# Performance work log

Hardware: AMD Instinct MI355X
Metric: run time of the kernel (lower is better)

Reference implementation:

```python
import jax, jax.numpy as jnp
import numpy as np

N, E, H, C = 50000, 800000, 4, 64
IN_DIM = 128
HID = H * C            # 256, concat output width
VH = C // 2            # 32, value-head hidden
OUT_DIM = 4
NEG_SLOPE = 0.2
LN_EPS = 1e-5


def setup_inputs() -> dict:
    key = jax.random.key(0)
    ks = iter(jax.random.split(key, 64))
    def nrm(shape, s=0.05):
        return jax.random.normal(next(ks), shape, jnp.float32) * s
    inp = {
        "x": jax.random.normal(next(ks), (N, IN_DIM), jnp.float32),
        "edge_src": jax.random.randint(next(ks), (E,), 0, N, dtype=jnp.int32),
        "edge_dst": jax.random.randint(next(ks), (E,), 0, N, dtype=jnp.int32),
        "proj_w": nrm((C, IN_DIM)),
        "proj_b": jnp.zeros((C,), jnp.float32),
    }
    in_dims = [C, HID, HID]
    out_feats = [HID, HID, C]
    for i in range(3):
        inp[f"w{i}"] = nrm((HID, in_dims[i]))
        inp[f"asrc{i}"] = nrm((H, C))
        inp[f"adst{i}"] = nrm((H, C))
        inp[f"b{i}"] = jnp.zeros((out_feats[i],), jnp.float32)
        inp[f"g{i}"] = jnp.ones((out_feats[i],), jnp.float32)
        inp[f"be{i}"] = jnp.zeros((out_feats[i],), jnp.float32)
    inp["vw1"] = nrm((VH, C)); inp["vb1"] = jnp.zeros((VH,), jnp.float32)
    inp["vw2"] = nrm((OUT_DIM, VH)); inp["vb2"] = jnp.zeros((OUT_DIM,), jnp.float32)
    return inp


def _layer_norm(x, g, b):
    mu = x.mean(-1, keepdims=True)
    var = ((x - mu) ** 2).mean(-1, keepdims=True)
    return (x - mu) * jax.lax.rsqrt(var + LN_EPS) * g + b


def _gat_conv(x, src, dst, w, a_s, a_d, bias, concat):
    # x: [N, in_dim] -> h: [N, H, C]
    n = x.shape[0]
    h = (x @ w.T).reshape(n, H, C)
    asrc = jnp.einsum('nhc,hc->nh', h, a_s)  # [N, H]
    adst = jnp.einsum('nhc,hc->nh', h, a_d)
    # PyG default add_self_loops=True
    loop = jnp.arange(n, dtype=src.dtype)
    src_f = jnp.concatenate([src, loop])
    dst_f = jnp.concatenate([dst, loop])
    alpha = jax.nn.leaky_relu(asrc[src_f] + adst[dst_f], NEG_SLOPE)  # [E+N, H]
    # segment softmax over incoming edges of each destination node
    amax = jax.ops.segment_max(alpha, dst_f, num_segments=n)
    ex = jnp.exp(alpha - amax[dst_f])
    denom = jax.ops.segment_sum(ex, dst_f, num_segments=n)
    coef = ex / (denom[dst_f] + 1e-16)
    out = jax.ops.segment_sum(h[src_f] * coef[:, :, None], dst_f, num_segments=n)
    out = out.reshape(n, H * C) if concat else out.mean(axis=1)
    return out + bias


def _gat_layer(x, src, dst, w, a_s, a_d, bias, g, be, concat):
    # GATConv -> LayerNorm -> ELU (dropout is identity in eval)
    return jax.nn.elu(_layer_norm(_gat_conv(x, src, dst, w, a_s, a_d, bias, concat), g, be))


def reference(x, edge_src, edge_dst, proj_w, proj_b,
              w0, asrc0, adst0, b0, g0, be0,
              w1, asrc1, adst1, b1, g1, be1,
              w2, asrc2, adst2, b2, g2, be2,
              vw1, vb1, vw2, vb2):
    h = jax.nn.elu(x @ proj_w.T + proj_b)
    h = _gat_layer(h, edge_src, edge_dst, w0, asrc0, adst0, b0, g0, be0, True)
    h = _gat_layer(h, edge_src, edge_dst, w1, asrc1, adst1, b1, g1, be1, True)
    h = _gat_layer(h, edge_src, edge_dst, w2, asrc2, adst2, b2, g2, be2, False)
    v = jax.nn.elu(h @ vw1.T + vb1)
    return v @ vw2.T + vb2
```

## Files before the change

### kernel.cpp

```cpp
#include <hip/hip_runtime.h>

typedef unsigned short u16;
typedef u16 u16x4 __attribute__((ext_vector_type(4)));
typedef short short8 __attribute__((ext_vector_type(8)));
typedef float f32x4 __attribute__((ext_vector_type(4)));

__device__ __forceinline__ float elu_f(float x) { return x > 0.f ? x : expm1f(x); }
__device__ __forceinline__ float lrelu_f(float x) { return x > 0.f ? x : 0.2f * x; }

__device__ __forceinline__ u16 f2b(float f) {
  union { float f; unsigned u; } v; v.f = f;
  unsigned r = v.u + 0x7FFF + ((v.u >> 16) & 1);
  return (u16)(r >> 16);
}
__device__ __forceinline__ float b2f(u16 u) {
  union { unsigned u; float f; } v; v.u = ((unsigned)u) << 16; return v.f;
}

__global__ void deg_count_k(const int* __restrict__ src, const int* __restrict__ dst,
                            int E, int n, int* __restrict__ deg) {
  int e = blockIdx.x * blockDim.x + threadIdx.x;
  if (e < E) {
    atomicAdd(&deg[dst[e]], 1);
  } else if (e < E + n) {
    atomicAdd(&deg[e - E], 1);
  }
}

__global__ __launch_bounds__(256) void block_sum_k(const int* __restrict__ deg,
                                                   int* __restrict__ bsum, int n) {
  int i = blockIdx.x * 256 + threadIdx.x;
  int v = (i < n) ? deg[i] : 0;
#pragma unroll
  for (int off = 1; off < 64; off <<= 1) v += __shfl_xor(v, off);
  __shared__ int ws[4];
  if ((threadIdx.x & 63) == 0) ws[threadIdx.x >> 6] = v;
  __syncthreads();
  if (threadIdx.x == 0) bsum[blockIdx.x] = ws[0] + ws[1] + ws[2] + ws[3];
}

__global__ void scan_bsum_k(int* __restrict__ bsum, int nb) {
  __shared__ int s[1024];
  int tid = threadIdx.x;
  int v = (tid < nb) ? bsum[tid] : 0;
  s[tid] = v;
  __syncthreads();
  for (int off = 1; off < 1024; off <<= 1) {
    int t = (tid >= off) ? s[tid - off] : 0;
    __syncthreads();
    s[tid] += t;
    __syncthreads();
  }
  if (tid < nb) bsum[tid] = s[tid] - v;
}

__global__ __launch_bounds__(256) void block_scan_k(const int* __restrict__ deg,
                                                    const int* __restrict__ bsum,
                                                    int* __restrict__ rowptr,
                                                    int* __restrict__ cursor, int n) {
  int i = blockIdx.x * 256 + threadIdx.x;
  int lane = threadIdx.x & 63, w = threadIdx.x >> 6;
  int v = (i < n) ? deg[i] : 0;
  int x = v;
#pragma unroll
  for (int off = 1; off < 64; off <<= 1) {
    int t = __shfl_up(x, off);
    if (lane >= off) x += t;
  }
  __shared__ int ws[4];
  if (lane == 63) ws[w] = x;
  __syncthreads();
  int add = bsum[blockIdx.x];
  for (int j = 0; j < w; ++j) add += ws[j];
  int excl = x - v + add;
  if (i < n) {
    cursor[i] = excl;
    rowptr[i + 1] = excl + v;
  }
  if (i == 0) rowptr[0] = 0;
}

__global__ void scatter_k(const int* __restrict__ src, const int* __restrict__ dst,
                          int E, int n, int* __restrict__ cursor,
                          int* __restrict__ col, int* __restrict__ dst2) {
  int e = blockIdx.x * blockDim.x + threadIdx.x;
  if (e < E) {
    int d = dst[e];
    int pos = atomicAdd(&cursor[d], 1);
    col[pos] = src[e];
    dst2[pos] = d;
  } else if (e < E + n) {
    int d = e - E;
    int pos = atomicAdd(&cursor[d], 1);
    col[pos] = d;
    dst2[pos] = d;
  }
}

__global__ __launch_bounds__(256) void cvt_all_k(const float* __restrict__ x, u16* __restrict__ xb,
                                                 int nx8,
                                                 const float* __restrict__ pw,
                                                 const float* __restrict__ w0,
                                                 const float* __restrict__ w1,
                                                 const float* __restrict__ w2,
                                                 u16* __restrict__ dp, u16* __restrict__ d0,
                                                 u16* __restrict__ d1, u16* __restrict__ d2) {
  int i = blockIdx.x * 256 + threadIdx.x;
  if (i < nx8) {
    int j = i * 8;
    float4 a = *reinterpret_cast<const float4*>(&x[j]);
    float4 b = *reinterpret_cast<const float4*>(&x[j + 4]);
    u16x4 o0, o1;
    o0.x = f2b(a.x); o0.y = f2b(a.y); o0.z = f2b(a.z); o0.w = f2b(a.w);
    o1.x = f2b(b.x); o1.y = f2b(b.y); o1.z = f2b(b.z); o1.w = f2b(b.w);
    *reinterpret_cast<u16x4*>(&xb[j]) = o0;
    *reinterpret_cast<u16x4*>(&xb[j + 4]) = o1;
  } else {
    int j = i - nx8;
    if (j < 8192) dp[j] = f2b(pw[j]);
    else if (j < 24576) d0[j - 8192] = f2b(w0[j - 8192]);
    else if (j < 90112) d1[j - 24576] = f2b(w1[j - 24576]);
    else if (j < 155648) d2[j - 90112] = f2b(w2[j - 90112]);
  }
}

template <int BIASELU>
__global__ __launch_bounds__(256) void gemm_bf16_k(const u16* __restrict__ A, int lda,
                                                   const u16* __restrict__ W,
                                                   const float* __restrict__ bias,
                                                   u16* __restrict__ Cb, int ldc,
                                                   int n, int K, int ncols) {
  __shared__ int4 Abuf[1024];
  __shared__ int4 Bbuf[1024];
  char* Asb = (char*)Abuf;
  char* Bsb = (char*)Bbuf;
  const int t = threadIdx.x;
  const int lane = t & 63, w = t >> 6;
  const int wrow = w >> 1, wcol = w & 1;
  const int row0 = blockIdx.x * 128, col0 = blockIdx.y * 128;
  f32x4 acc[4][4];
#pragma unroll
  for (int m = 0; m < 4; ++m)
#pragma unroll
    for (int nf = 0; nf < 4; ++nf) acc[m][nf] = (f32x4){0.f, 0.f, 0.f, 0.f};

  for (int k0 = 0; k0 < K; k0 += 64) {
#pragma unroll
    for (int i = 0; i < 4; ++i) {
      int ci = i * 256 + t;
      int r = ci >> 3;
      int b = (ci & 7) << 4;
      int sw = b ^ ((r & 7) << 4);
      int ar = row0 + r; ar = ar < n ? ar : n - 1;
      int4 av = *reinterpret_cast<const int4*>(&A[(size_t)ar * lda + k0 + (b >> 1)]);
      *reinterpret_cast<int4*>(Asb + r * 128 + sw) = av;
      int wr = col0 + r; wr = wr < ncols ? wr : ncols - 1;
      int4 wv = *reinterpret_cast<const int4*>(&W[(size_t)wr * K + k0 + (b >> 1)]);
      *reinterpret_cast<int4*>(Bsb + r * 128 + sw) = wv;
    }
    __syncthreads();
#pragma unroll
    for (int ks = 0; ks < 2; ++ks) {
      short8 af[4], bf[4];
      int kb = ks * 64 + ((lane >> 4) << 4);
#pragma unroll
      for (int m = 0; m < 4; ++m) {
        int r = wrow * 64 + m * 16 + (lane & 15);
        af[m] = *reinterpret_cast<const short8*>(Asb + r * 128 + (kb ^ ((r & 7) << 4)));
      }
#pragma unroll
      for (int nf = 0; nf < 4; ++nf) {
        int r = wcol * 64 + nf * 16 + (lane & 15);
        bf[nf] = *reinterpret_cast<const short8*>(Bsb + r * 128 + (kb ^ ((r & 7) << 4)));
      }
#pragma unroll
      for (int m = 0; m < 4; ++m)
#pragma unroll
        for (int nf = 0; nf < 4; ++nf)
          acc[m][nf] = __builtin_amdgcn_mfma_f32_16x16x32_bf16(af[m], bf[nf], acc[m][nf], 0, 0, 0);
    }
    __syncthreads();
  }
#pragma unroll
  for (int m = 0; m < 4; ++m) {
#pragma unroll
    for (int j = 0; j < 4; ++j) {
      int rg = row0 + wrow * 64 + m * 16 + (lane >> 4) * 4 + j;
      if (rg >= n) continue;
#pragma unroll
      for (int nf = 0; nf < 4; ++nf) {
        int cg = col0 + wcol * 64 + nf * 16 + (lane & 15);
        if (cg >= ncols) continue;
        float v = acc[m][nf][j];
        if (BIASELU) v = elu_f(v + bias[cg]);
        Cb[(size_t)rg * ldc + cg] = f2b(v);
      }
    }
  }
}

__global__ __launch_bounds__(512) void gemm2_k(const u16* __restrict__ A, int lda,
                                               const u16* __restrict__ W,
                                               u16* __restrict__ Cb,
                                               int n, int K,
                                               const float* __restrict__ a_sv,
                                               const float* __restrict__ a_dv,
                                               float* __restrict__ asrcN,
                                               float* __restrict__ adstN) {
  __shared__ char Asb[128 * 128];
  __shared__ char Bsb[256 * 128];
  const int t = threadIdx.x;
  const int lane = t & 63, w = t >> 6;
  const int wrow = w >> 2, wcol = w & 3;
  const int row0 = blockIdx.x * 128;
  f32x4 acc[4][4];
#pragma unroll
  for (int m = 0; m < 4; ++m)
#pragma unroll
    for (int nf = 0; nf < 4; ++nf) acc[m][nf] = (f32x4){0.f, 0.f, 0.f, 0.f};

  for (int k0 = 0; k0 < K; k0 += 64) {
#pragma unroll
    for (int i = 0; i < 2; ++i) {
      int ci = i * 512 + t;
      int r = ci >> 3;
      int b = (ci & 7) << 4;
      int sw = b ^ ((r & 7) << 4);
      int ar = row0 + r; ar = ar < n ? ar : n - 1;
      int4 av = *reinterpret_cast<const int4*>(&A[(size_t)ar * lda + k0 + (b >> 1)]);
      *reinterpret_cast<int4*>(Asb + r * 128 + sw) = av;
    }
#pragma unroll
    for (int i = 0; i < 4; ++i) {
      int ci = i * 512 + t;
      int r = ci >> 3;
      int b = (ci & 7) << 4;
      int sw = b ^ ((r & 7) << 4);
      int4 wv = *reinterpret_cast<const int4*>(&W[(size_t)r * K + k0 + (b >> 1)]);
      *reinterpret_cast<int4*>(Bsb + r * 128 + sw) = wv;
    }
    __syncthreads();
#pragma unroll
    for (int ks = 0; ks < 2; ++ks) {
      short8 af[4], bf[4];
      int kb = ks * 64 + ((lane >> 4) << 4);
#pragma unroll
      for (int m = 0; m < 4; ++m) {
        int r = wrow * 64 + m * 16 + (lane & 15);
        af[m] = *reinterpret_cast<const short8*>(Asb + r * 128 + (kb ^ ((r & 7) << 4)));
      }
#pragma unroll
      for (int nf = 0; nf < 4; ++nf) {
        int r = wcol * 64 + nf * 16 + (lane & 15);
        bf[nf] = *reinterpret_cast<const short8*>(Bsb + r * 128 + (kb ^ ((r & 7) << 4)));
      }
#pragma unroll
      for (int m = 0; m < 4; ++m)
#pragma unroll
        for (int nf = 0; nf < 4; ++nf)
          acc[m][nf] = __builtin_amdgcn_mfma_f32_16x16x32_bf16(af[m], bf[nf], acc[m][nf], 0, 0, 0);
    }
    __syncthreads();
  }
#pragma unroll
  for (int m = 0; m < 4; ++m) {
#pragma unroll
    for (int j = 0; j < 4; ++j) {
      int rg = row0 + wrow * 64 + m * 16 + (lane >> 4) * 4 + j;
      if (rg >= n) continue;
#pragma unroll
      for (int nf = 0; nf < 4; ++nf) {
        int cg = wcol * 64 + nf * 16 + (lane & 15);
        Cb[(size_t)rg * 256 + cg] = f2b(acc[m][nf][j]);
      }
    }
  }
  {
    int h = wcol;
    int ch = lane & 15;
    float as_c[4], ad_c[4];
#pragma unroll
    for (int nf = 0; nf < 4; ++nf) {
      as_c[nf] = a_sv[h * 64 + nf * 16 + ch];
      ad_c[nf] = a_dv[h * 64 + nf * 16 + ch];
    }
#pragma unroll
    for (int m = 0; m < 4; ++m) {
#pragma unroll
      for (int j = 0; j < 4; ++j) {
        float ps = 0.f, pd = 0.f;
#pragma unroll
        for (int nf = 0; nf < 4; ++nf) {
          float v = acc[m][nf][j];
          ps += v * as_c[nf];
          pd += v * ad_c[nf];
        }
#pragma unroll
        for (int off = 1; off < 16; off <<= 1) {
          ps += __shfl_xor(ps, off);
          pd += __shfl_xor(pd, off);
        }
        int rg = row0 + wrow * 64 + m * 16 + (lane >> 4) * 4 + j;
        if ((lane & 15) == 0 && rg < n) {
          asrcN[(size_t)rg * 4 + h] = ps;
          adstN[(size_t)rg * 4 + h] = pd;
        }
      }
    }
  }
}

__global__ __launch_bounds__(256) void edge_ex2_k(const int* __restrict__ col,
                                                  const int* __restrict__ dst2,
                                                  const float* __restrict__ asrcN,
                                                  const float* __restrict__ adstN,
                                                  float* __restrict__ exT, int eep, int EE) {
  int e = blockIdx.x * 256 + threadIdx.x;
  if (e >= EE) return;
  int s = col[e], d = dst2[e];
  float4 as = *reinterpret_cast<const float4*>(&asrcN[(size_t)s * 4]);
  float4 ad = *reinterpret_cast<const float4*>(&adstN[(size_t)d * 4]);
  exT[e]            = __expf(lrelu_f(as.x + ad.x));
  exT[eep + e]      = __expf(lrelu_f(as.y + ad.y));
  exT[2 * eep + e]  = __expf(lrelu_f(as.z + ad.z));
  exT[3 * eep + e]  = __expf(lrelu_f(as.w + ad.w));
}

template <int MODE>
__global__ __launch_bounds__(256) void gat_agg4_k(const u16* __restrict__ feat,
                                                  const float* __restrict__ exT, int eep,
                                                  const int* __restrict__ rowptr,
                                                  const int* __restrict__ col,
                                                  const float* __restrict__ bias,
                                                  const float* __restrict__ g,
                                                  const float* __restrict__ be,
                                                  void* __restrict__ out, int n) {
  int wave = threadIdx.x >> 6, lane = threadIdx.x & 63;
  int node = blockIdx.x * 4 + wave;
  if (node >= n) return;
  int h = lane >> 4;
  const float* exh = exT + (size_t)h * eep;
  int s0 = rowptr[node], s1 = rowptr[node + 1];
  float ax = 0.f, ay = 0.f, az = 0.f, aw = 0.f, den = 0.f;
  int e = s0;
  for (; e + 8 <= s1; e += 8) {
    int p0 = col[e + 0], p1 = col[e + 1], p2 = col[e + 2], p3 = col[e + 3];
    int q0 = col[e + 4], q1 = col[e + 5], q2 = col[e + 6], q3 = col[e + 7];
    float u0 = exh[e + 0], u1 = exh[e + 1], u2 = exh[e + 2], u3 = exh[e + 3];
    float v0 = exh[e + 4], v1 = exh[e + 5], v2 = exh[e + 6], v3 = exh[e + 7];
    u16x4 fp0 = *reinterpret_cast<const u16x4*>(&feat[(size_t)p0 * 256 + lane * 4]);
    u16x4 fp1 = *reinterpret_cast<const u16x4*>(&feat[(size_t)p1 * 256 + lane * 4]);
    u16x4 fp2 = *reinterpret_cast<const u16x4*>(&feat[(size_t)p2 * 256 + lane * 4]);
    u16x4 fp3 = *reinterpret_cast<const u16x4*>(&feat[(size_t)p3 * 256 + lane * 4]);
    u16x4 fq0 = *reinterpret_cast<const u16x4*>(&feat[(size_t)q0 * 256 + lane * 4]);
    u16x4 fq1 = *reinterpret_cast<const u16x4*>(&feat[(size_t)q1 * 256 + lane * 4]);
    u16x4 fq2 = *reinterpret_cast<const u16x4*>(&feat[(size_t)q2 * 256 + lane * 4]);
    u16x4 fq3 = *reinterpret_cast<const u16x4*>(&feat[(size_t)q3 * 256 + lane * 4]);
    den += ((u0 + u1) + (u2 + u3)) + ((v0 + v1) + (v2 + v3));
    ax += u0 * b2f(fp0.x) + u1 * b2f(fp1.x) + u2 * b2f(fp2.x) + u3 * b2f(fp3.x);
    ay += u0 * b2f(fp0.y) + u1 * b2f(fp1.y) + u2 * b2f(fp2.y) + u3 * b2f(fp3.y);
    az += u0 * b2f(fp0.z) + u1 * b2f(fp1.z) + u2 * b2f(fp2.z) + u3 * b2f(fp3.z);
    aw += u0 * b2f(fp0.w) + u1 * b2f(fp1.w) + u2 * b2f(fp2.w) + u3 * b2f(fp3.w);
    ax += v0 * b2f(fq0.x) + v1 * b2f(fq1.x) + v2 * b2f(fq2.x) + v3 * b2f(fq3.x);
    ay += v0 * b2f(fq0.y) + v1 * b2f(fq1.y) + v2 * b2f(fq2.y) + v3 * b2f(fq3.y);
    az += v0 * b2f(fq0.z) + v1 * b2f(fq1.z) + v2 * b2f(fq2.z) + v3 * b2f(fq3.z);
    aw += v0 * b2f(fq0.w) + v1 * b2f(fq1.w) + v2 * b2f(fq2.w) + v3 * b2f(fq3.w);
  }
  for (; e + 4 <= s1; e += 4) {
    int p0 = col[e + 0], p1 = col[e + 1], p2 = col[e + 2], p3 = col[e + 3];
    float u0 = exh[e + 0], u1 = exh[e + 1], u2 = exh[e + 2], u3 = exh[e + 3];
    u16x4 fp0 = *reinterpret_cast<const u16x4*>(&feat[(size_t)p0 * 256 + lane * 4]);
    u16x4 fp1 = *reinterpret_cast<const u16x4*>(&feat[(size_t)p1 * 256 + lane * 4]);
    u16x4 fp2 = *reinterpret_cast<const u16x4*>(&feat[(size_t)p2 * 256 + lane * 4]);
    u16x4 fp3 = *reinterpret_cast<const u16x4*>(&feat[(size_t)p3 * 256 + lane * 4]);
    den += (u0 + u1) + (u2 + u3);
    ax += u0 * b2f(fp0.x) + u1 * b2f(fp1.x) + u2 * b2f(fp2.x) + u3 * b2f(fp3.x);
    ay += u0 * b2f(fp0.y) + u1 * b2f(fp1.y) + u2 * b2f(fp2.y) + u3 * b2f(fp3.y);
    az += u0 * b2f(fp0.z) + u1 * b2f(fp1.z) + u2 * b2f(fp2.z) + u3 * b2f(fp3.z);
    aw += u0 * b2f(fp0.w) + u1 * b2f(fp1.w) + u2 * b2f(fp2.w) + u3 * b2f(fp3.w);
  }
  for (; e < s1; ++e) {
    int s = col[e];
    float x = exh[e];
    den += x;
    u16x4 f = *reinterpret_cast<const u16x4*>(&feat[(size_t)s * 256 + lane * 4]);
    ax += x * b2f(f.x); ay += x * b2f(f.y); az += x * b2f(f.z); aw += x * b2f(f.w);
  }
  float inv = 1.f / den;
  ax *= inv; ay *= inv; az *= inv; aw *= inv;

  if (MODE == 0) {
    float4 b4 = *reinterpret_cast<const float4*>(&bias[lane * 4]);
    float vx = ax + b4.x, vy = ay + b4.y, vz = az + b4.z, vw = aw + b4.w;
    float s = vx + vy + vz + vw;
#pragma unroll
    for (int off = 1; off < 64; off <<= 1) s += __shfl_xor(s, off);
    float mu = s * (1.f / 256.f);
    float dx = vx - mu, dy = vy - mu, dz = vz - mu, dw = vw - mu;
    float q = dx * dx + dy * dy + dz * dz + dw * dw;
#pragma unroll
    for (int off = 1; off < 64; off <<= 1) q += __shfl_xor(q, off);
    float inv2 = rsqrtf(q * (1.f / 256.f) + 1e-5f);
    float4 gg = *reinterpret_cast<const float4*>(&g[lane * 4]);
    float4 bb = *reinterpret_cast<const float4*>(&be[lane * 4]);
    u16x4 o;
    o.x = f2b(elu_f(dx * inv2 * gg.x + bb.x));
    o.y = f2b(elu_f(dy * inv2 * gg.y + bb.y));
    o.z = f2b(elu_f(dz * inv2 * gg.z + bb.z));
    o.w = f2b(elu_f(dw * inv2 * gg.w + bb.w));
    u16* rowb = (u16*)out + (size_t)node * 256;
    *reinterpret_cast<u16x4*>(&rowb[lane * 4]) = o;
  } else {
    ax += __shfl_xor(ax, 16); ax += __shfl_xor(ax, 32);
    ay += __shfl_xor(ay, 16); ay += __shfl_xor(ay, 32);
    az += __shfl_xor(az, 16); az += __shfl_xor(az, 32);
    aw += __shfl_xor(aw, 16); aw += __shfl_xor(aw, 32);
    int qd = lane & 15;
    float4 b4 = *reinterpret_cast<const float4*>(&bias[qd * 4]);
    float vx = 0.25f * ax + b4.x, vy = 0.25f * ay + b4.y;
    float vz = 0.25f * az + b4.z, vw = 0.25f * aw + b4.w;
    float s = vx + vy + vz + vw;
#pragma unroll
    for (int off = 1; off < 64; off <<= 1) s += __shfl_xor(s, off);
    float mu = s * (1.f / 256.f);
    float dx = vx - mu, dy = vy - mu, dz = vz - mu, dw = vw - mu;
    float q = dx * dx + dy * dy + dz * dz + dw * dw;
#pragma unroll
    for (int off = 1; off < 64; off <<= 1) q += __shfl_xor(q, off);
    float inv2 = rsqrtf(q * (1.f / 256.f) + 1e-5f);
    if (lane < 16) {
      float4 gg = *reinterpret_cast<const float4*>(&g[qd * 4]);
      float4 bb = *reinterpret_cast<const float4*>(&be[qd * 4]);
      float4 o;
      o.x = elu_f(dx * inv2 * gg.x + bb.x);
      o.y = elu_f(dy * inv2 * gg.y + bb.y);
      o.z = elu_f(dz * inv2 * gg.z + bb.z);
      o.w = elu_f(dw * inv2 * gg.w + bb.w);
      *reinterpret_cast<float4*>(&((float*)out)[(size_t)node * 64 + qd * 4]) = o;
    }
  }
}

__global__ __launch_bounds__(256) void value_head_k(const float* __restrict__ hh,
                                                    const float* __restrict__ vw1,
                                                    const float* __restrict__ vb1,
                                                    const float* __restrict__ vw2,
                                                    const float* __restrict__ vb2,
                                                    float* __restrict__ out, int n) {
  __shared__ float w1s[32 * 65];
  __shared__ float hs[4][64];
  __shared__ float vs[4][33];
  int tid = threadIdx.x;
  for (int i = tid; i < 2048; i += 256) w1s[(i >> 6) * 65 + (i & 63)] = vw1[i];
  int wave = tid >> 6, lane = tid & 63;
  int node = blockIdx.x * 4 + wave;
  int nc = node < n ? node : n - 1;
  hs[wave][lane] = hh[(size_t)nc * 64 + lane];
  __syncthreads();
  int j = lane & 31, half = lane >> 5;
  float p = 0.f;
#pragma unroll
  for (int c = 0; c < 32; ++c) p += hs[wave][half * 32 + c] * w1s[j * 65 + half * 32 + c];
  p += __shfl_xor(p, 32);
  float v = elu_f(p + vb1[j]);
  if (half == 0) vs[wave][j] = v;
  __syncthreads();
  if (lane < 4 && node < n) {
    float o = vb2[lane];
#pragma unroll
    for (int jj = 0; jj < 32; ++jj) o += vs[wave][jj] * vw2[lane * 32 + jj];
    out[(size_t)node * 4 + lane] = o;
  }
}

extern "C" void kernel_launch(void* const* d_in, const int* in_sizes, int n_in,
                              void* d_out, int out_size, void* d_ws, size_t ws_size,
                              hipStream_t stream) {
  const float* x      = (const float*)d_in[0];
  const int*   esrc   = (const int*)d_in[1];
  const int*   edst   = (const int*)d_in[2];
  const float* proj_w = (const float*)d_in[3];
  const float* proj_b = (const float*)d_in[4];
  const float* w[3]   = {(const float*)d_in[5],  (const float*)d_in[11], (const float*)d_in[17]};
  const float* a_s[3] = {(const float*)d_in[6],  (const float*)d_in[12], (const float*)d_in[18]};
  const float* a_d[3] = {(const float*)d_in[7],  (const float*)d_in[13], (const float*)d_in[19]};
  const float* bb[3]  = {(const float*)d_in[8],  (const float*)d_in[14], (const float*)d_in[20]};
  const float* gg[3]  = {(const float*)d_in[9],  (const float*)d_in[15], (const float*)d_in[21]};
  const float* be[3]  = {(const float*)d_in[10], (const float*)d_in[16], (const float*)d_in[22]};
  const float* vw1 = (const float*)d_in[23];
  const float* vb1 = (const float*)d_in[24];
  const float* vw2 = (const float*)d_in[25];
  const float* vb2 = (const float*)d_in[26];
  float* outp = (float*)d_out;

  const int n = in_sizes[0] / 128;
  const int E = in_sizes[1];
  const int EE = E + n;
  const int eep = (EE + 255) & ~255;
  const int nbl = (n + 255) / 256;

  char* p = (char*)d_ws;
  auto alloc = [&](size_t bytes) { char* r = p; p += (bytes + 255) & ~(size_t)255; return r; };
  u16*   hA    = (u16*)alloc((size_t)n * 512);
  u16*   featB = (u16*)alloc((size_t)n * 512);
  float* exT   = (float*)alloc((size_t)eep * 16);
  float* asrcN = (float*)alloc((size_t)n * 16);
  float* adstN = (float*)alloc((size_t)n * 16);
  u16* wbp = (u16*)alloc(64 * 128 * 2);
  u16* wb[3];
  wb[0] = (u16*)alloc(256 * 64 * 2);
  wb[1] = (u16*)alloc(256 * 256 * 2);
  wb[2] = (u16*)alloc(256 * 256 * 2);
  int* deg    = (int*)alloc((size_t)n * 4);
  int* rowptr = (int*)alloc((size_t)(n + 1) * 4);
  int* cursor = (int*)alloc((size_t)n * 4);
  int* col    = (int*)alloc((size_t)EE * 4);
  int* dst2   = (int*)alloc((size_t)EE * 4);
  int* bsum   = (int*)alloc((size_t)nbl * 4);
  float* hfinal = (float*)hA;

  hipMemsetAsync(deg, 0, (size_t)n * sizeof(int), stream);
  deg_count_k<<<(EE + 255) / 256, 256, 0, stream>>>(esrc, edst, E, n, deg);
  block_sum_k<<<nbl, 256, 0, stream>>>(deg, bsum, n);
  scan_bsum_k<<<1, 1024, 0, stream>>>(bsum, nbl);
  block_scan_k<<<nbl, 256, 0, stream>>>(deg, bsum, rowptr, cursor, n);
  scatter_k<<<(EE + 255) / 256, 256, 0, stream>>>(esrc, edst, E, n, cursor, col, dst2);

  const int nx8 = n * 16;
  cvt_all_k<<<(nx8 + 155648 + 255) / 256, 256, 0, stream>>>(x, featB, nx8, proj_w, w[0], w[1], w[2],
                                                            wbp, wb[0], wb[1], wb[2]);

  const int nb4 = (n + 3) / 4;
  const int nbg = (n + 127) / 128;
  dim3 blk(256);

  gemm_bf16_k<1><<<dim3(nbg, 1), blk, 0, stream>>>(featB, 128, wbp, proj_b, hA, 256, n, 128, 64);

  const int Kin[3] = {64, 256, 256};
  for (int i = 0; i < 3; ++i) {
    gemm2_k<<<nbg, 512, 0, stream>>>(hA, 256, wb[i], featB, n, Kin[i],
                                     a_s[i], a_d[i], asrcN, adstN);
    edge_ex2_k<<<(EE + 255) / 256, 256, 0, stream>>>(col, dst2, asrcN, adstN, exT, eep, EE);
    if (i < 2) {
      gat_agg4_k<0><<<nb4, blk, 0, stream>>>(featB, exT, eep, rowptr, col, bb[i], gg[i], be[i], (void*)hA, n);
    } else {
      gat_agg4_k<1><<<nb4, blk, 0, stream>>>(featB, exT, eep, rowptr, col, bb[i], gg[i], be[i], (void*)hfinal, n);
    }
  }

  value_head_k<<<nb4, blk, 0, stream>>>(hfinal, vw1, vb1, vw2, vb2, outp, n);
}
```

Before: 426.1 us.

## Fuse input projection into first GAT GEMM, value head into last aggregation

The degree-count atomics now run inside the conversion kernel, which removes one launch. The input projection GEMM with bias and ELU is computed inside the layer-0 gemm2 kernel, and its bf16 result is written straight into the swizzled A tile in LDS. This avoids a global round trip of the projected features. The value-head MLP is folded into the final aggregation kernel's epilogue using wave shuffles, which removes the fp32 hfinal write/read and a separate launch. The cost is more LDS and register use in the fused kernels.

Result: faster. 400.0 us (-6.1%).

```diff
diff --git a/kernel.cpp b/kernel.cpp
--- a/kernel.cpp
+++ b/kernel.cpp
@@ -17,13 +17,36 @@
   union { unsigned u; float f; } v; v.u = ((unsigned)u) << 16; return v.f;
 }
 
-__global__ void deg_count_k(const int* __restrict__ src, const int* __restrict__ dst,
-                            int E, int n, int* __restrict__ deg) {
-  int e = blockIdx.x * blockDim.x + threadIdx.x;
-  if (e < E) {
-    atomicAdd(&deg[dst[e]], 1);
-  } else if (e < E + n) {
-    atomicAdd(&deg[e - E], 1);
+__global__ __launch_bounds__(256) void cvtdeg_k(const float* __restrict__ x, u16* __restrict__ xb,
+                                                int nx8,
+                                                const float* __restrict__ pw,
+                                                const float* __restrict__ w0,
+                                                const float* __restrict__ w1,
+                                                const float* __restrict__ w2,
+                                                u16* __restrict__ dp, u16* __restrict__ d0,
+                                                u16* __restrict__ d1, u16* __restrict__ d2,
+                                                const int* __restrict__ edst,
+                                                int E, int n, int* __restrict__ deg) {
+  int i = blockIdx.x * 256 + threadIdx.x;
+  if (i < nx8) {
+    int j = i * 8;
+    float4 a = *reinterpret_cast<const float4*>(&x[j]);
+    float4 b = *reinterpret_cast<const float4*>(&x[j + 4]);
+    u16x4 o0, o1;
+    o0.x = f2b(a.x); o0.y = f2b(a.y); o0.z = f2b(a.z); o0.w = f2b(a.w);
+    o1.x = f2b(b.x); o1.y = f2b(b.y); o1.z = f2b(b.z); o1.w = f2b(b.w);
+    *reinterpret_cast<u16x4*>(&xb[j]) = o0;
+    *reinterpret_cast<u16x4*>(&xb[j + 4]) = o1;
+  } else if (i < nx8 + 155648) {
+    int j = i - nx8;
+    if (j < 8192) dp[j] = f2b(pw[j]);
+    else if (j < 24576) d0[j - 8192] = f2b(w0[j - 8192]);
+    else if (j < 90112) d1[j - 24576] = f2b(w1[j - 24576]);
+    else d2[j - 90112] = f2b(w2[j - 90112]);
+  } else {
+    int j = i - (nx8 + 155648);
+    if (j < E) atomicAdd(&deg[edst[j]], 1);
+    else if (j < E + n) atomicAdd(&deg[j - E], 1);
   }
 }
 
@@ -97,110 +120,11 @@
   }
 }
 
-__global__ __launch_bounds__(256) void cvt_all_k(const float* __restrict__ x, u16* __restrict__ xb,
-                                                 int nx8,
-                                                 const float* __restrict__ pw,
-                                                 const float* __restrict__ w0,
-                                                 const float* __restrict__ w1,
-                                                 const float* __restrict__ w2,
-                                                 u16* __restrict__ dp, u16* __restrict__ d0,
-                                                 u16* __restrict__ d1, u16* __restrict__ d2) {
-  int i = blockIdx.x * 256 + threadIdx.x;
-  if (i < nx8) {
-    int j = i * 8;
-    float4 a = *reinterpret_cast<const float4*>(&x[j]);
-    float4 b = *reinterpret_cast<const float4*>(&x[j + 4]);
-    u16x4 o0, o1;
-    o0.x = f2b(a.x); o0.y = f2b(a.y); o0.z = f2b(a.z); o0.w = f2b(a.w);
-    o1.x = f2b(b.x); o1.y = f2b(b.y); o1.z = f2b(b.z); o1.w = f2b(b.w);
-    *reinterpret_cast<u16x4*>(&xb[j]) = o0;
-    *reinterpret_cast<u16x4*>(&xb[j + 4]) = o1;
-  } else {
-    int j = i - nx8;
-    if (j < 8192) dp[j] = f2b(pw[j]);
-    else if (j < 24576) d0[j - 8192] = f2b(w0[j - 8192]);
-    else if (j < 90112) d1[j - 24576] = f2b(w1[j - 24576]);
-    else if (j < 155648) d2[j - 90112] = f2b(w2[j - 90112]);
-  }
-}
-
-template <int BIASELU>
-__global__ __launch_bounds__(256) void gemm_bf16_k(const u16* __restrict__ A, int lda,
-                                                   const u16* __restrict__ W,
-                                                   const float* __restrict__ bias,
-                                                   u16* __restrict__ Cb, int ldc,
-                                                   int n, int K, int ncols) {
-  __shared__ int4 Abuf[1024];
-  __shared__ int4 Bbuf[1024];
-  char* Asb = (char*)Abuf;
-  char* Bsb = (char*)Bbuf;
-  const int t = threadIdx.x;
-  const int lane = t & 63, w = t >> 6;
-  const int wrow = w >> 1, wcol = w & 1;
-  const int row0 = blockIdx.x * 128, col0 = blockIdx.y * 128;
-  f32x4 acc[4][4];
-#pragma unroll
-  for (int m = 0; m < 4; ++m)
-#pragma unroll
-    for (int nf = 0; nf < 4; ++nf) acc[m][nf] = (f32x4){0.f, 0.f, 0.f, 0.f};
-
-  for (int k0 = 0; k0 < K; k0 += 64) {
-#pragma unroll
-    for (int i = 0; i < 4; ++i) {
-      int ci = i * 256 + t;
-      int r = ci >> 3;
-      int b = (ci & 7) << 4;
-      int sw = b ^ ((r & 7) << 4);
-      int ar = row0 + r; ar = ar < n ? ar : n - 1;
-      int4 av = *reinterpret_cast<const int4*>(&A[(size_t)ar * lda + k0 + (b >> 1)]);
-      *reinterpret_cast<int4*>(Asb + r * 128 + sw) = av;
-      int wr = col0 + r; wr = wr < ncols ? wr : ncols - 1;
-      int4 wv = *reinterpret_cast<const int4*>(&W[(size_t)wr * K + k0 + (b >> 1)]);
-      *reinterpret_cast<int4*>(Bsb + r * 128 + sw) = wv;
-    }
-    __syncthreads();
-#pragma unroll
-    for (int ks = 0; ks < 2; ++ks) {
-      short8 af[4], bf[4];
-      int kb = ks * 64 + ((lane >> 4) << 4);
-#pragma unroll
-      for (int m = 0; m < 4; ++m) {
-        int r = wrow * 64 + m * 16 + (lane & 15);
-        af[m] = *reinterpret_cast<const short8*>(Asb + r * 128 + (kb ^ ((r & 7) << 4)));
-      }
-#pragma unroll
-      for (int nf = 0; nf < 4; ++nf) {
-        int r = wcol * 64 + nf * 16 + (lane & 15);
-        bf[nf] = *reinterpret_cast<const short8*>(Bsb + r * 128 + (kb ^ ((r & 7) << 4)));
-      }
-#pragma unroll
-      for (int m = 0; m < 4; ++m)
-#pragma unroll
-        for (int nf = 0; nf < 4; ++nf)
-          acc[m][nf] = __builtin_amdgcn_mfma_f32_16x16x32_bf16(af[m], bf[nf], acc[m][nf], 0, 0, 0);
-    }
-    __syncthreads();
-  }
-#pragma unroll
-  for (int m = 0; m < 4; ++m) {
-#pragma unroll
-    for (int j = 0; j < 4; ++j) {
-      int rg = row0 + wrow * 64 + m * 16 + (lane >> 4) * 4 + j;
-      if (rg >= n) continue;
-#pragma unroll
-      for (int nf = 0; nf < 4; ++nf) {
-        int cg = col0 + wcol * 64 + nf * 16 + (lane & 15);
-        if (cg >= ncols) continue;
-        float v = acc[m][nf][j];
-        if (BIASELU) v = elu_f(v + bias[cg]);
-        Cb[(size_t)rg * ldc + cg] = f2b(v);
-      }
-    }
-  }
-}
-
+template <int PROJ>
 __global__ __launch_bounds__(512) void gemm2_k(const u16* __restrict__ A, int lda,
                                                const u16* __restrict__ W,
+                                               const u16* __restrict__ pw,
+                                               const float* __restrict__ pb,
                                                u16* __restrict__ Cb,
                                                int n, int K,
                                                const float* __restrict__ a_sv,
@@ -209,26 +133,76 @@
                                                float* __restrict__ adstN) {
   __shared__ char Asb[128 * 128];
   __shared__ char Bsb[256 * 128];
+  __shared__ char Xsb[PROJ ? 128 * 272 : 16];
+  __shared__ char Psb[PROJ ? 64 * 272 : 16];
   const int t = threadIdx.x;
   const int lane = t & 63, w = t >> 6;
   const int wrow = w >> 2, wcol = w & 3;
   const int row0 = blockIdx.x * 128;
-  f32x4 acc[4][4];
-#pragma unroll
-  for (int m = 0; m < 4; ++m)
-#pragma unroll
-    for (int nf = 0; nf < 4; ++nf) acc[m][nf] = (f32x4){0.f, 0.f, 0.f, 0.f};
-
-  for (int k0 = 0; k0 < K; k0 += 64) {
+
+  if (PROJ) {
+#pragma unroll
+    for (int i = 0; i < 4; ++i) {
+      int ci = i * 512 + t;
+      int r = ci >> 4;
+      int b = (ci & 15) << 4;
+      int ar = row0 + r; ar = ar < n ? ar : n - 1;
+      *reinterpret_cast<int4*>(Xsb + r * 272 + b) =
+          *reinterpret_cast<const int4*>(&A[(size_t)ar * 128 + (b >> 1)]);
+    }
 #pragma unroll
     for (int i = 0; i < 2; ++i) {
       int ci = i * 512 + t;
-      int r = ci >> 3;
-      int b = (ci & 7) << 4;
-      int sw = b ^ ((r & 7) << 4);
-      int ar = row0 + r; ar = ar < n ? ar : n - 1;
-      int4 av = *reinterpret_cast<const int4*>(&A[(size_t)ar * lda + k0 + (b >> 1)]);
-      *reinterpret_cast<int4*>(Asb + r * 128 + sw) = av;
+      int r = ci >> 4;
+      int b = (ci & 15) << 4;
+      *reinterpret_cast<int4*>(Psb + r * 272 + b) =
+          *reinterpret_cast<const int4*>(&pw[r * 128 + (b >> 1)]);
+    }
+    __syncthreads();
+    f32x4 pacc[4];
+#pragma unroll
+    for (int nf = 0; nf < 4; ++nf) pacc[nf] = (f32x4){0.f, 0.f, 0.f, 0.f};
+#pragma unroll
+    for (int ks = 0; ks < 4; ++ks) {
+      short8 paf = *reinterpret_cast<const short8*>(
+          Xsb + (w * 16 + (lane & 15)) * 272 + ks * 64 + (lane >> 4) * 16);
+#pragma unroll
+      for (int nf = 0; nf < 4; ++nf) {
+        short8 pbf = *reinterpret_cast<const short8*>(
+            Psb + (nf * 16 + (lane & 15)) * 272 + ks * 64 + (lane >> 4) * 16);
+        pacc[nf] = __builtin_amdgcn_mfma_f32_16x16x32_bf16(paf, pbf, pacc[nf], 0, 0, 0);
+      }
+    }
+#pragma unroll
+    for (int nf = 0; nf < 4; ++nf) {
+#pragma unroll
+      for (int j = 0; j < 4; ++j) {
+        int rl = w * 16 + (lane >> 4) * 4 + j;
+        int cg = nf * 16 + (lane & 15);
+        u16 bv = f2b(elu_f(pacc[nf][j] + pb[cg]));
+        *reinterpret_cast<u16*>(Asb + rl * 128 + ((cg * 2) ^ ((rl & 7) << 4))) = bv;
+      }
+    }
+  }
+
+  f32x4 acc[4][4];
+#pragma unroll
+  for (int m = 0; m < 4; ++m)
+#pragma unroll
+    for (int nf = 0; nf < 4; ++nf) acc[m][nf] = (f32x4){0.f, 0.f, 0.f, 0.f};
+
+  for (int k0 = 0; k0 < K; k0 += 64) {
+    if (!PROJ) {
+#pragma unroll
+      for (int i = 0; i < 2; ++i) {
+        int ci = i * 512 + t;
+        int r = ci >> 3;
+        int b = (ci & 7) << 4;
+        int sw = b ^ ((r & 7) << 4);
+        int ar = row0 + r; ar = ar < n ? ar : n - 1;
+        int4 av = *reinterpret_cast<const int4*>(&A[(size_t)ar * lda + k0 + (b >> 1)]);
+        *reinterpret_cast<int4*>(Asb + r * 128 + sw) = av;
+      }
     }
 #pragma unroll
     for (int i = 0; i < 4; ++i) {
@@ -334,6 +308,10 @@
                                                   const float* __restrict__ bias,
                                                   const float* __restrict__ g,
                                                   const float* __restrict__ be,
+                                                  const float* __restrict__ vw1,
+                                                  const float* __restrict__ vb1,
+                                                  const float* __restrict__ vw2,
+                                                  const float* __restrict__ vb2,
                                                   void* __restrict__ out, int n) {
   int wave = threadIdx.x >> 6, lane = threadIdx.x & 63;
   int node = blockIdx.x * 4 + wave;
@@ -381,10 +359,10 @@
   }
   for (; e < s1; ++e) {
     int s = col[e];
-    float x = exh[e];
-    den += x;
+    float xv = exh[e];
+    den += xv;
     u16x4 f = *reinterpret_cast<const u16x4*>(&feat[(size_t)s * 256 + lane * 4]);
-    ax += x * b2f(f.x); ay += x * b2f(f.y); az += x * b2f(f.z); aw += x * b2f(f.w);
+    ax += xv * b2f(f.x); ay += xv * b2f(f.y); az += xv * b2f(f.z); aw += xv * b2f(f.w);
   }
   float inv = 1.f / den;
   ax *= inv; ay *= inv; az *= inv; aw *= inv;
@@ -428,48 +406,51 @@
 #pragma unroll
     for (int off = 1; off < 64; off <<= 1) q += __shfl_xor(q, off);
     float inv2 = rsqrtf(q * (1.f / 256.f) + 1e-5f);
-    if (lane < 16) {
-      float4 gg = *reinterpret_cast<const float4*>(&g[qd * 4]);
-      float4 bb = *reinterpret_cast<const float4*>(&be[qd * 4]);
-      float4 o;
-      o.x = elu_f(dx * inv2 * gg.x + bb.x);
-      o.y = elu_f(dy * inv2 * gg.y + bb.y);
-      o.z = elu_f(dz * inv2 * gg.z + bb.z);
-      o.w = elu_f(dw * inv2 * gg.w + bb.w);
-      *reinterpret_cast<float4*>(&((float*)out)[(size_t)node * 64 + qd * 4]) = o;
-    }
-  }
-}
-
-__global__ __launch_bounds__(256) void value_head_k(const float* __restrict__ hh,
-                                                    const float* __restrict__ vw1,
-                                                    const float* __restrict__ vb1,
-                                                    const float* __restrict__ vw2,
-                                                    const float* __restrict__ vb2,
-                                                    float* __restrict__ out, int n) {
-  __shared__ float w1s[32 * 65];
-  __shared__ float hs[4][64];
-  __shared__ float vs[4][33];
-  int tid = threadIdx.x;
-  for (int i = tid; i < 2048; i += 256) w1s[(i >> 6) * 65 + (i & 63)] = vw1[i];
-  int wave = tid >> 6, lane = tid & 63;
-  int node = blockIdx.x * 4 + wave;
-  int nc = node < n ? node : n - 1;
-  hs[wave][lane] = hh[(size_t)nc * 64 + lane];
-  __syncthreads();
-  int j = lane & 31, half = lane >> 5;
-  float p = 0.f;
-#pragma unroll
-  for (int c = 0; c < 32; ++c) p += hs[wave][half * 32 + c] * w1s[j * 65 + half * 32 + c];
-  p += __shfl_xor(p, 32);
-  float v = elu_f(p + vb1[j]);
-  if (half == 0) vs[wave][j] = v;
-  __syncthreads();
-  if (lane < 4 && node < n) {
-    float o = vb2[lane];
-#pragma unroll
-    for (int jj = 0; jj < 32; ++jj) o += vs[wave][jj] * vw2[lane * 32 + jj];
-    out[(size_t)node * 4 + lane] = o;
+    float4 gg = *reinterpret_cast<const float4*>(&g[qd * 4]);
+    float4 bb = *reinterpret_cast<const float4*>(&be[qd * 4]);
+    float h0 = elu_f(dx * inv2 * gg.x + bb.x);
+    float h1 = elu_f(dy * inv2 * gg.y + bb.y);
+    float h2 = elu_f(dz * inv2 * gg.z + bb.z);
+    float h3 = elu_f(dw * inv2 * gg.w + bb.w);
+    int r = (lane >> 4) & 3;
+    float pj[8];
+#pragma unroll
+    for (int jj = 0; jj < 8; ++jj) {
+      int j = r * 8 + jj;
+      float4 wv = *reinterpret_cast<const float4*>(&vw1[(size_t)j * 64 + qd * 4]);
+      pj[jj] = h0 * wv.x + h1 * wv.y + h2 * wv.z + h3 * wv.w;
+    }
+#pragma unroll
+    for (int off = 1; off < 16; off <<= 1) {
+#pragma unroll
+      for (int jj = 0; jj < 8; ++jj) pj[jj] += __shfl_xor(pj[jj], off);
+    }
+    float4 vb1a = *reinterpret_cast<const float4*>(&vb1[r * 8]);
+    float4 vb1b = *reinterpret_cast<const float4*>(&vb1[r * 8 + 4]);
+    float vj0 = elu_f(pj[0] + vb1a.x), vj1 = elu_f(pj[1] + vb1a.y);
+    float vj2 = elu_f(pj[2] + vb1a.z), vj3 = elu_f(pj[3] + vb1a.w);
+    float vj4 = elu_f(pj[4] + vb1b.x), vj5 = elu_f(pj[5] + vb1b.y);
+    float vj6 = elu_f(pj[6] + vb1b.z), vj7 = elu_f(pj[7] + vb1b.w);
+    float qo[4];
+#pragma unroll
+    for (int o = 0; o < 4; ++o) {
+      float4 w2a = *reinterpret_cast<const float4*>(&vw2[o * 32 + r * 8]);
+      float4 w2b = *reinterpret_cast<const float4*>(&vw2[o * 32 + r * 8 + 4]);
+      qo[o] = vj0 * w2a.x + vj1 * w2a.y + vj2 * w2a.z + vj3 * w2a.w +
+              vj4 * w2b.x + vj5 * w2b.y + vj6 * w2b.z + vj7 * w2b.w;
+    }
+#pragma unroll
+    for (int o = 0; o < 4; ++o) {
+      qo[o] += __shfl_xor(qo[o], 16);
+      qo[o] += __shfl_xor(qo[o], 32);
+    }
+    if (lane == 0) {
+      float4 vb2v = *reinterpret_cast<const float4*>(&vb2[0]);
+      float4 o4;
+      o4.x = qo[0] + vb2v.x; o4.y = qo[1] + vb2v.y;
+      o4.z = qo[2] + vb2v.z; o4.w = qo[3] + vb2v.w;
+      *reinterpret_cast<float4*>(&((float*)out)[(size_t)node * 4]) = o4;
+    }
   }
 }
 
@@ -503,6 +484,7 @@
   auto alloc = [&](size_t bytes) { char* r = p; p += (bytes + 255) & ~(size_t)255; return r; };
   u16*   hA    = (u16*)alloc((size_t)n * 512);
   u16*   featB = (u16*)alloc((size_t)n * 512);
+  u16*   xb    = (u16*)alloc((size_t)n * 256);
   float* exT   = (float*)alloc((size_t)eep * 16);
   float* asrcN = (float*)alloc((size_t)n * 16);
   float* adstN = (float*)alloc((size_t)n * 16);
@@ -517,36 +499,36 @@
   int* col    = (int*)alloc((size_t)EE * 4);
   int* dst2   = (int*)alloc((size_t)EE * 4);
   int* bsum   = (int*)alloc((size_t)nbl * 4);
-  float* hfinal = (float*)hA;
 
   hipMemsetAsync(deg, 0, (size_t)n * sizeof(int), stream);
-  deg_count_k<<<(EE + 255) / 256, 256, 0, stream>>>(esrc, edst, E, n, deg);
+  const int nx8 = n * 16;
+  cvtdeg_k<<<(nx8 + 155648 + EE + 255) / 256, 256, 0, stream>>>(
+      x, xb, nx8, proj_w, w[0], w[1], w[2], wbp, wb[0], wb[1], wb[2], edst, E, n, deg);
   block_sum_k<<<nbl, 256, 0, stream>>>(deg, bsum, n);
   scan_bsum_k<<<1, 1024, 0, stream>>>(bsum, nbl);
   block_scan_k<<<nbl, 256, 0, stream>>>(deg, bsum, rowptr, cursor, n);
   scatter_k<<<(EE + 255) / 256, 256, 0, stream>>>(esrc, edst, E, n, cursor, col, dst2);
 
-  const int nx8 = n * 16;
-  cvt_all_k<<<(nx8 + 155648 + 255) / 256, 256, 0, stream>>>(x, featB, nx8, proj_w, w[0], w[1], w[2],
-                                                            wbp, wb[0], wb[1], wb[2]);
-
   const int nb4 = (n + 3) / 4;
   const int nbg = (n + 127) / 128;
   dim3 blk(256);
 
-  gemm_bf16_k<1><<<dim3(nbg, 1), blk, 0, stream>>>(featB, 128, wbp, proj_b, hA, 256, n, 128, 64);
-
   const int Kin[3] = {64, 256, 256};
   for (int i = 0; i < 3; ++i) {
-    gemm2_k<<<nbg, 512, 0, stream>>>(hA, 256, wb[i], featB, n, Kin[i],
-                                     a_s[i], a_d[i], asrcN, adstN);
+    if (i == 0) {
+      gemm2_k<1><<<nbg, 512, 0, stream>>>(xb, 128, wb[0], wbp, proj_b, featB,
+                                          n, 64, a_s[0], a_d[0], asrcN, adstN);
+    } else {
+      gemm2_k<0><<<nbg, 512, 0, stream>>>(hA, 256, wb[i], nullptr, nullptr, featB,
+                                          n, Kin[i], a_s[i], a_d[i], asrcN, adstN);
+    }
     edge_ex2_k<<<(EE + 255) / 256, 256, 0, stream>>>(col, dst2, asrcN, adstN, exT, eep, EE);
     if (i < 2) {
-      gat_agg4_k<0><<<nb4, blk, 0, stream>>>(featB, exT, eep, rowptr, col, bb[i], gg[i], be[i], (void*)hA, n);
+      gat_agg4_k<0><<<nb4, blk, 0, stream>>>(featB, exT, eep, rowptr, col, bb[i], gg[i], be[i],
+                                             nullptr, nullptr, nullptr, nullptr, (void*)hA, n);
     } else {
-      gat_agg4_k<1><<<nb4, blk, 0, stream>>>(featB, exT, eep, rowptr, col, bb[i], gg[i], be[i], (void*)hfinal, n);
-    }
-  }
-
-  value_head_k<<<nb4, blk, 0, stream>>>(hfinal, vw1, vb1, vw2, vb2, outp, n);
-}
+      gat_agg4_k<1><<<nb4, blk, 0, stream>>>(featB, exT, eep, rowptr, col, bb[i], gg[i], be[i],
+                                             vw1, vb1, vw2, vb2, (void*)outp, n);
+    }
+  }
+}
```
